# Optimization experiments

Hardware: AMD Instinct MI355X
Metric: run time of the kernel (lower is better)

The kernel has to match this reference:

```python
import jax, jax.numpy as jnp
import numpy as np

NX = 48
NY = 48
K0DX = 0.2026833935483871
N_PML = 8
_PI = 3.1415926


def _fun_s(u):
    # PML stretch factor s(u) = kappa(u) + 1j*sigma_over_omega(u)
    power_kappa = 3
    kappa_max = 15
    power_sigma = 3
    lambda_over_dx = 40
    sigma_over_omega_max = 0.8 * (power_sigma + 1) * lambda_over_dx / (2 * _PI)
    return (1.0 + (kappa_max - 1) * u ** power_kappa) + 1j * (sigma_over_omega_max * u ** power_sigma)


def _lap1d_pml(N, N_L, N_R):
    # 1D second-difference operator with stretched-coordinate PML (dense numpy, constant)
    ddx1 = np.eye(N + 1, N) - np.eye(N + 1, N, k=-1)   # forward difference (N+1, N)
    ddx2 = -ddx1.T                                      # (N, N+1)
    s_half = np.ones(N + 1, dtype=np.complex128)
    s_int = np.ones(N, dtype=np.complex128)
    if N_R > 0:
        s_half[N - N_R:N + 1] = _fun_s(np.arange(0.5, N_R + 1, 1.0) / (N_R + 1))
        s_int[N - N_R:N] = _fun_s(np.arange(1.0, N_R + 1, 1.0) / (N_R + 1))
    if N_L > 0:
        s_half[N_L::-1] = _fun_s(np.arange(0.5, N_L + 1, 1.0) / (N_L + 1))
        s_int[N_L - 1::-1] = _fun_s(np.arange(1.0, N_L + 1, 1.0) / (N_L + 1))
    return np.diag(1.0 / s_int) @ ddx2 @ np.diag(1.0 / s_half) @ ddx1


def _build_A1():
    # 2D Helmholtz Laplacian with PML: kron(Ax, I) + kron(I, Ay), dense 2304x2304 complex64
    Ax = _lap1d_pml(NX, N_PML, N_PML)
    Ay = _lap1d_pml(NY, N_PML, N_PML)
    return (np.kron(Ax, np.eye(NY)) + np.kron(np.eye(NX), Ay)).astype(np.complex64)


_A1 = _build_A1()  # constant system matrix part


def setup_inputs() -> dict:
    key = jax.random.key(0)
    k1, k2, k3, k4, k5 = jax.random.split(key, 5)
    return {
        "n_prediction": jax.random.uniform(k1, (1, NX, NY, 1), dtype=jnp.float32),
        "n_predict_allresults": jax.random.normal(k2, (1, NX, NY, 1), dtype=jnp.float32),
        "x_b": jax.random.normal(k3, (1, NX, NY, 1), dtype=jnp.float32),
        "y_aim": jax.random.normal(k4, (1, NX, NY, 2), dtype=jnp.float32),
        "simulation_region": jax.random.normal(k5, (1, NX, NY, 1), dtype=jnp.float32),
    }


def reference(n_prediction, n_predict_allresults, x_b, y_aim, simulation_region):
    A1 = jnp.asarray(_A1)  # (2304, 2304) complex64
    # A = A1 + k0dx^2 * diag(n^2), with n flattened after [0,2,1,3] transpose
    n_c = n_prediction.astype(jnp.complex64)
    n_flat = jnp.transpose(n_c, (0, 2, 1, 3)).reshape(-1)  # (2304,)
    A = A1 + jnp.diag((K0DX ** 2) * n_flat ** 2)
    # RHS b, same transpose+flatten convention
    b = jnp.transpose(x_b.astype(jnp.complex64), (0, 2, 1, 3)).reshape(NX * NY, 1)
    # Dense complex linear solve A psi = b
    psi = jnp.linalg.solve(A, b).reshape(1, NX, NY, 1)
    psi_tot = jnp.transpose(psi, (0, 2, 1, 3))  # (1, 48, 48, 1) complex64
    y_c = y_aim.astype(jnp.complex64)
    err1 = psi_tot * y_c[:, :, :, 0:1]
    err2 = psi_tot * y_c[:, :, :, 1:2]
    en1 = y_c[:, :, :, 0:1] * y_c[:, :, :, 0:1]
    en2 = y_c[:, :, :, 1:2] * y_c[:, :, :, 1:2]
    return jnp.concatenate([err1, err2, en1, en2], axis=-1)  # (1, 48, 48, 4) complex64
```

## Files before the change

### kernel.cpp

```cpp
#include <hip/hip_runtime.h>


#define NXY 48
#define NN  2304

typedef float v2 __attribute__((ext_vector_type(2)));
typedef double2 zplx;

__device__ __forceinline__ v2 mk2(float x, float y){ v2 r; r.x=x; r.y=y; return r; }
__device__ __forceinline__ v2 bcx(v2 a){ return __builtin_shufflevector(a,a,0,0); }
__device__ __forceinline__ v2 bcy(v2 a){ return __builtin_shufflevector(a,a,1,1); }
__device__ __forceinline__ v2 jswp(v2 a){ v2 r = __builtin_shufflevector(a,a,1,0); r.x = -r.x; return r; }
__device__ __forceinline__ v2 cmul(v2 a, v2 b){
    return __builtin_elementwise_fma(bcx(a), b, bcy(a)*jswp(b));
}
__device__ __forceinline__ v2 cfma_(v2 c, v2 a, v2 b){
    return __builtin_elementwise_fma(bcx(a), b, __builtin_elementwise_fma(bcy(a), jswp(b), c));
}
__device__ __forceinline__ v2 cfms(v2 c, v2 a, v2 b){
    return __builtin_elementwise_fma(-bcx(a), b, __builtin_elementwise_fma(-bcy(a), jswp(b), c));
}
__device__ __forceinline__ v2 cinv(v2 a){
    float s = 1.0f/fmaf(a.x,a.x, a.y*a.y);
    return mk2(a.x*s, -a.y*s);
}
__device__ __forceinline__ v2 shfl_c(v2 a, int lane){
    return mk2(__shfl(a.x, lane), __shfl(a.y, lane));
}
__device__ __forceinline__ v2 bfly_c(v2 v){
    v.x += __shfl_xor(v.x,1); v.y += __shfl_xor(v.y,1);
    v.x += __shfl_xor(v.x,2); v.y += __shfl_xor(v.y,2);
    v.x += __shfl_xor(v.x,4); v.y += __shfl_xor(v.y,4);
    return v;
}

__device__ __forceinline__ zplx zmul64(zplx a, zplx b){
    return make_double2(a.x*b.x - a.y*b.y, a.x*b.y + a.y*b.x);
}
__device__ __forceinline__ zplx zadd64(zplx a, zplx b){ return make_double2(a.x+b.x, a.y+b.y); }
__device__ __forceinline__ zplx zneg64(zplx a){ return make_double2(-a.x, -a.y); }
__device__ __forceinline__ zplx zinv64(zplx a){
    double s = 1.0/(a.x*a.x + a.y*a.y);
    return make_double2(a.x*s, -a.y*s);
}
__device__ __forceinline__ zplx fun_s(double u){
    const double sig = 0.8*4.0*40.0/(2.0*3.1415926);
    double u3 = u*u*u;
    return make_double2(1.0 + 14.0*u3, sig*u3);
}
__device__ __forceinline__ zplx s_half_at(int j){
    if (j <= 8)  return fun_s((8.5 - (double)j)/9.0);
    if (j >= 40) return fun_s(((double)(j-40) + 0.5)/9.0);
    return make_double2(1.0, 0.0);
}
__device__ __forceinline__ zplx s_int_at(int j){
    if (j <= 7)  return fun_s((8.0 - (double)j)/9.0);
    if (j >= 40) return fun_s(((double)(j-40) + 1.0)/9.0);
    return make_double2(1.0, 0.0);
}

__device__ __forceinline__ void gj48(v2 (&m)[6][6], const int lr, const int lc){
    v2 pv, rs[6], cs[6];
    {
        const int rsrc0 = lc, csrc0 = (lr<<3);
        pv = shfl_c(m[0][0], 0);
        #pragma unroll
        for (int j=0;j<6;++j) rs[j] = shfl_c(m[0][j], rsrc0);
        #pragma unroll
        for (int i=0;i<6;++i) cs[i] = shfl_c(m[i][0], csrc0);
    }
    #pragma unroll 1
    for (int kr=0; kr<8; ++kr){
        const bool prow = (lr==kr), pcol = (lc==kr);
        #pragma unroll
        for (int kj=0; kj<6; ++kj){
            const int nj = (kj+1)%6;
            const int cr = (kj==5) ? ((kr<7)?(kr+1):7) : kr;
            const int nrsrc = (cr<<3)|lc;
            const int ncsrc = (lr<<3)|cr;
            const int ndsrc = (cr<<3)|cr;
            v2 d = cinv(pv);
            v2 rsp[6];
            #pragma unroll
            for (int j=0;j<6;++j) rsp[j] = cmul(d, rs[j]);
            if (pcol) rsp[kj] = d + mk2(1.f,0.f);
            v2 u[6];
            #pragma unroll
            for (int i=0;i<6;++i) u[i] = cs[i];
            if (prow) u[kj] = pv - mk2(1.f,0.f);
            #pragma unroll
            for (int j=0;j<6;++j) m[nj][j] = cfms(m[nj][j], u[nj], rsp[j]);
            #pragma unroll
            for (int i=0;i<6;++i){ if (i!=nj) m[i][nj] = cfms(m[i][nj], u[i], rsp[nj]); }
            v2 npv = shfl_c(m[nj][nj], ndsrc);
            v2 nrs[6], ncs[6];
            #pragma unroll
            for (int j=0;j<6;++j) nrs[j] = shfl_c(m[nj][j], nrsrc);
            #pragma unroll
            for (int i=0;i<6;++i) ncs[i] = shfl_c(m[i][nj], ncsrc);
            #pragma unroll
            for (int i=0;i<6;++i){
                if (i==nj) continue;
                #pragma unroll
                for (int j=0;j<6;++j){
                    if (j==nj) continue;
                    m[i][j] = cfms(m[i][j], u[i], rsp[j]);
                }
            }
            pv = npv;
            #pragma unroll
            for (int j=0;j<6;++j){ rs[j]=nrs[j]; cs[j]=ncs[j]; }
        }
    }
}

__global__ __launch_bounds__(128,1) void helm_babe(
    const float* __restrict__ n_pred,
    const float* __restrict__ xb,
    const float* __restrict__ yaim,
    float*       __restrict__ out,
    int                       out_size,
    float*       __restrict__ wsG)
{
    __shared__ v2 dgv[NXY], lov[NXY], hiv[NXY];
    __shared__ float nk[NN];
    __shared__ float bb[NN];
    __shared__ v2 zv[NN];
    __shared__ v2 Hx[NN];
    __shared__ v2 vv[NXY];

    const int t    = threadIdx.x;
    const int lane = t & 63;
    const int wid  = t >> 6;
    const int lr = lane>>3, lc = lane&7;
    const int r0 = 6*lr, c0v = 6*lc;
    const int diagl = (lc<<3)|lc;
    const double k2 = 0.2026833935483871*0.2026833935483871;

    if (t < NXY){
        int a = t;
        zplx isha  = zinv64(s_half_at(a));
        zplx isha1 = zinv64(s_half_at(a+1));
        zplx isi   = zinv64(s_int_at(a));
        zplx dgd = zneg64(zmul64(isi, zadd64(isha,isha1)));
        zplx lod = zmul64(isi, isha);
        zplx hid = zmul64(isi, isha1);
        dgv[a] = mk2((float)dgd.x,(float)dgd.y);
        lov[a] = mk2((float)lod.x,(float)lod.y);
        hiv[a] = mk2((float)hid.x,(float)hid.y);
    }
    for (int e=t; e<NN; e+=128){
        int i_=e/48, a_=e%48;
        float nv = n_pred[a_*48+i_];
        nk[e] = (float)(k2*(double)nv*(double)nv);
        bb[e] = xb[a_*48+i_];
    }
    __syncthreads();

    const int dir    = (wid==0) ? 1 : -1;
    const int ibeg   = (wid==0) ? 0 : 47;
    const int nsteps = (wid==0) ? 25 : 23;

    v2 g[6][6];
    v2 m[6][6];
    v2 zrow[6];
    #pragma unroll
    for (int i=0;i<6;++i) zrow[i] = mk2(0.f,0.f);

    #pragma unroll 1
    for (int step=0; step<nsteps; ++step){
        int ib = ibeg + dir*step;
        bool full = !(wid==0 && step==24);

        v2 zc[6];
        #pragma unroll
        for (int j=0;j<6;++j) zc[j] = shfl_c(zrow[j], diagl);

        v2 nci = mk2(0.f,0.f), czp = mk2(0.f,0.f);
        if (step>0){
            if (dir>0){ nci = cmul(lov[ib], hiv[ib-1]); czp = lov[ib]; }
            else      { nci = cmul(hiv[ib], lov[ib+1]); czp = hiv[ib]; }
            nci = -nci;
        }
        bool same  = (lc==lr), rightn = (lc==lr+1), leftn = (lc+1==lr);
        v2 p[6];
        #pragma unroll
        for (int i=0;i<6;++i){
            int r = r0+i;
            v2 dgr = dgv[r], lor = lov[r], hir = hiv[r];
            v2 ddi = dgv[ib] + dgr + mk2(nk[ib*48+r],0.f);
            v2 acc = mk2(0.f,0.f);
            #pragma unroll
            for (int j=0;j<6;++j){
                v2 v = (step>0)? cmul(nci, g[i][j]) : mk2(0.f,0.f);
                if (same){
                    if (j==i)   v = v + ddi;
                    if (j==i+1) v = v + hir;
                    if (j+1==i) v = v + lor;
                }
                if (rightn && i==5 && j==0) v = v + hir;
                if (leftn  && i==0 && j==5) v = v + lor;
                m[i][j] = v;
                if (step>0) acc = cfma_(acc, g[i][j], zc[j]);
            }
            p[i] = acc;
        }
        if (step>0){
            #pragma unroll
            for (int i=0;i<6;++i){
                v2 w = bfly_c(p[i]);
                zrow[i] = cfms(mk2(bb[ib*48+r0+i],0.f), czp, w);
            }
        } else {
            #pragma unroll
            for (int i=0;i<6;++i) zrow[i] = mk2(bb[ib*48+r0+i], 0.f);
        }
        if (lc==0){
            #pragma unroll
            for (int i=0;i<6;++i) zv[ib*48+r0+i] = zrow[i];
        }

        if (full){
            gj48(m, lr, lc);
            if (ib == 25){
                #pragma unroll
                for (int i=0;i<6;++i)
                    #pragma unroll
                    for (int j=0;j<6;++j) Hx[(r0+i)*48 + c0v + j] = m[i][j];
            } else {
                #pragma unroll
                for (int i=0;i<6;++i){
                    float4* w4 = (float4*)(wsG + 2*((size_t)ib*NN + (r0+i)*48 + c0v));
                    #pragma unroll
                    for (int jp=0;jp<3;++jp){
                        float4 f;
                        f.x = m[i][2*jp].x;   f.y = m[i][2*jp].y;
                        f.z = m[i][2*jp+1].x; f.w = m[i][2*jp+1].y;
                        w4[jp] = f;
                    }
                }
            }
            #pragma unroll
            for (int i=0;i<6;++i)
                #pragma unroll
                for (int j=0;j<6;++j) g[i][j] = m[i][j];
        }
    }

    if (wid==1){
        v2 zc[6];
        #pragma unroll
        for (int j=0;j<6;++j) zc[j] = shfl_c(zrow[j], diagl);
        #pragma unroll
        for (int i=0;i<6;++i){
            v2 acc = mk2(0.f,0.f);
            #pragma unroll
            for (int j=0;j<6;++j) acc = cfma_(acc, m[i][j], zc[j]);
            acc = bfly_c(acc);
            if (lc==0) vv[r0+i] = acc;
        }
    }
    __syncthreads();

    v2 xrow[6];
    if (wid==0){
        v2 cf = cmul(hiv[24], lov[25]);
        #pragma unroll
        for (int i=0;i<6;++i)
            #pragma unroll
            for (int j=0;j<6;++j) m[i][j] = cfms(m[i][j], cf, Hx[(r0+i)*48 + c0v + j]);
        #pragma unroll
        for (int i=0;i<6;++i) zrow[i] = cfms(zrow[i], hiv[24], vv[r0+i]);
        gj48(m, lr, lc);
        v2 zc[6];
        #pragma unroll
        for (int j=0;j<6;++j) zc[j] = shfl_c(zrow[j], diagl);
        #pragma unroll
        for (int i=0;i<6;++i){
            v2 acc = mk2(0.f,0.f);
            #pragma unroll
            for (int j=0;j<6;++j) acc = cfma_(acc, m[i][j], zc[j]);
            xrow[i] = bfly_c(acc);
        }
        if (lc==0){
            #pragma unroll
            for (int i=0;i<6;++i) zv[24*48+r0+i] = xrow[i];
        }
        v2 xc[6], tm[6];
        #pragma unroll
        for (int j=0;j<6;++j) xc[j] = shfl_c(xrow[j], diagl);
        #pragma unroll
        for (int j=0;j<6;++j) tm[j] = cfms(zv[25*48+c0v+j], lov[25], xc[j]);
        #pragma unroll
        for (int i=0;i<6;++i){
            v2 acc = mk2(0.f,0.f);
            #pragma unroll
            for (int j=0;j<6;++j) acc = cfma_(acc, Hx[(r0+i)*48 + c0v + j], tm[j]);
            acc = bfly_c(acc);
            if (lc==0) zv[25*48+r0+i] = acc;
        }
    }
    __syncthreads();

    if (wid==0){
        #pragma unroll 1
        for (int ib=23; ib>=0; --ib){
            v2 xc[6], tm[6];
            #pragma unroll
            for (int j=0;j<6;++j) xc[j] = shfl_c(xrow[j], diagl);
            v2 hiib = hiv[ib];
            #pragma unroll
            for (int j=0;j<6;++j) tm[j] = cfms(zv[ib*48+c0v+j], hiib, xc[j]);
            #pragma unroll
            for (int i=0;i<6;++i){
                const float4* w4 = (const float4*)(wsG + 2*((size_t)ib*NN + (r0+i)*48 + c0v));
                v2 acc = mk2(0.f,0.f);
                #pragma unroll
                for (int jp=0;jp<3;++jp){
                    float4 f = w4[jp];
                    acc = cfma_(acc, mk2(f.x,f.y), tm[2*jp]);
                    acc = cfma_(acc, mk2(f.z,f.w), tm[2*jp+1]);
                }
                xrow[i] = bfly_c(acc);
            }
            if (lc==0){
                #pragma unroll
                for (int i=0;i<6;++i) zv[ib*48+r0+i] = xrow[i];
            }
        }
    } else {
        #pragma unroll
        for (int i=0;i<6;++i) xrow[i] = zv[25*48+r0+i];
        #pragma unroll 1
        for (int ib=26; ib<NXY; ++ib){
            v2 xc[6], tm[6];
            #pragma unroll
            for (int j=0;j<6;++j) xc[j] = shfl_c(xrow[j], diagl);
            v2 loib = lov[ib];
            #pragma unroll
            for (int j=0;j<6;++j) tm[j] = cfms(zv[ib*48+c0v+j], loib, xc[j]);
            #pragma unroll
            for (int i=0;i<6;++i){
                const float4* w4 = (const float4*)(wsG + 2*((size_t)ib*NN + (r0+i)*48 + c0v));
                v2 acc = mk2(0.f,0.f);
                #pragma unroll
                for (int jp=0;jp<3;++jp){
                    float4 f = w4[jp];
                    acc = cfma_(acc, mk2(f.x,f.y), tm[2*jp]);
                    acc = cfma_(acc, mk2(f.z,f.w), tm[2*jp+1]);
                }
                xrow[i] = bfly_c(acc);
            }
            if (lc==0){
                #pragma unroll
                for (int i=0;i<6;++i) zv[ib*48+r0+i] = xrow[i];
            }
        }
    }
    __syncthreads();

    for (int e=t; e<NN; e+=128){
        int alpha=e/48, beta=e%48;
        v2 psi = zv[beta*48+alpha];
        float y0=yaim[2*e], y1=yaim[2*e+1];
        if (out_size == NN*4){
            float4 o = make_float4(psi.x*y0, psi.x*y1, y0*y0, y1*y1);
            *(float4*)(out + 4*e) = o;
        } else {
            float* o = out + 8*e;
            o[0]=psi.x*y0; o[1]=psi.y*y0; o[2]=psi.x*y1; o[3]=psi.y*y1;
            o[4]=y0*y0; o[5]=0.f; o[6]=y1*y1; o[7]=0.f;
        }
    }
}

extern "C" void kernel_launch(void* const* d_in, const int* in_sizes, int n_in,
                              void* d_out, int out_size, void* d_ws, size_t ws_size,
                              hipStream_t stream) {
    const float* n_pred = (const float*)d_in[0];
    const float* xb     = (const float*)d_in[2];
    const float* ya     = (const float*)d_in[3];
    float* out = (float*)d_out;
    float* wsG = (float*)d_ws;

    hipLaunchKernelGGL(helm_babe, dim3(1), dim3(128), 0, stream,
                       n_pred, xb, ya, out, out_size, wsG);
}
```

Baseline: 615.5 us.

## Block Gauss-Jordan 48x48 inversion with 2x2 pivot blocks

Replaces the scalar-pivot in-register Gauss-Jordan inversion with a 2x2 block-pivot version. Each step eliminates two pivot rows and columns together using an explicit 2x2 inverse, which halves the number of sequential pivot steps and the cross-lane shuffle/broadcast rounds on the critical path. The cost is more arithmetic per step, higher register pressure from the doubled row and column buffers, and pivoting on 2x2 determinants without pivot search, which may change numerical stability.

```diff
diff --git a/kernel.cpp b/kernel.cpp
--- a/kernel.cpp
+++ b/kernel.cpp
@@ -14,6 +14,9 @@
 __device__ __forceinline__ v2 cmul(v2 a, v2 b){
     return __builtin_elementwise_fma(bcx(a), b, bcy(a)*jswp(b));
 }
+__device__ __forceinline__ v2 cadd(v2 a, v2 b){ return a+b; }
+__device__ __forceinline__ v2 csub(v2 a, v2 b){ return a-b; }
+__device__ __forceinline__ v2 cneg(v2 a){ return -a; }
 __device__ __forceinline__ v2 cfma_(v2 c, v2 a, v2 b){
     return __builtin_elementwise_fma(bcx(a), b, __builtin_elementwise_fma(bcy(a), jswp(b), c));
 }
@@ -33,6 +36,9 @@
     v.x += __shfl_xor(v.x,4); v.y += __shfl_xor(v.y,4);
     return v;
 }
+__device__ __forceinline__ float4 pk4(v2 a, v2 b){ return make_float4(a.x,a.y,b.x,b.y); }
+__device__ __forceinline__ v2 lo2(float4 f){ return mk2(f.x,f.y); }
+__device__ __forceinline__ v2 hi2(float4 f){ return mk2(f.z,f.w); }
 
 __device__ __forceinline__ zplx zmul64(zplx a, zplx b){
     return make_double2(a.x*b.x - a.y*b.y, a.x*b.y + a.y*b.x);
@@ -59,58 +65,99 @@
     return make_double2(1.0, 0.0);
 }
 
-__device__ __forceinline__ void gj48(v2 (&m)[6][6], const int lr, const int lc){
-    v2 pv, rs[6], cs[6];
-    {
-        const int rsrc0 = lc, csrc0 = (lr<<3);
-        pv = shfl_c(m[0][0], 0);
-        #pragma unroll
-        for (int j=0;j<6;++j) rs[j] = shfl_c(m[0][j], rsrc0);
-        #pragma unroll
-        for (int i=0;i<6;++i) cs[i] = shfl_c(m[i][0], csrc0);
-    }
+template<int NI>
+__device__ __forceinline__ void gather_pair(const v2 (&m)[6][6], int gkr, int lr, int lc,
+    v2 (&rs0)[6], v2 (&rs1)[6], v2 (&cs0)[6], v2 (&cs1)[6],
+    v2 &P00, v2 &P01, v2 &P10, v2 &P11)
+{
+    const int rsrc = (gkr<<3)|lc;
+    const int csrc = (lr<<3)|gkr;
+    const int dsrc = (gkr<<3)|gkr;
+    #pragma unroll
+    for (int j=0;j<6;++j){ rs0[j] = shfl_c(m[NI][j], rsrc); rs1[j] = shfl_c(m[NI+1][j], rsrc); }
+    #pragma unroll
+    for (int i=0;i<6;++i){ cs0[i] = shfl_c(m[i][NI], csrc); cs1[i] = shfl_c(m[i][NI+1], csrc); }
+    P00 = shfl_c(m[NI][NI],   dsrc); P01 = shfl_c(m[NI][NI+1],   dsrc);
+    P10 = shfl_c(m[NI+1][NI], dsrc); P11 = shfl_c(m[NI+1][NI+1], dsrc);
+}
+
+#define UPD(i,j) m[i][j] = cfms(cfms(m[i][j], u0[i], rsp0[j]), u1[i], rsp1[j])
+
+template<int KJ2>
+__device__ __forceinline__ void gjb2_phase(v2 (&m)[6][6], const int kr, const bool last,
+    const int lr, const int lc,
+    v2 (&rs0)[6], v2 (&rs1)[6], v2 (&cs0)[6], v2 (&cs1)[6],
+    v2 &P00, v2 &P01, v2 &P10, v2 &P11)
+{
+    constexpr int iA = 2*KJ2, iB = iA+1;
+    constexpr int niA = 2*((KJ2+1)%3), niB = niA+1;
+    const int nkr = (KJ2==2)? kr+1 : kr;
+    const bool prow = (lr==kr), pcol = (lc==kr);
+
+    v2 det  = csub(cmul(P00,P11), cmul(P01,P10));
+    v2 dinv = cinv(det);
+    v2 D00 = cmul(P11,dinv);
+    v2 D01 = cneg(cmul(P01,dinv));
+    v2 D10 = cneg(cmul(P10,dinv));
+    v2 D11 = cmul(P00,dinv);
+
+    v2 u0[6], u1[6];
+    #pragma unroll
+    for (int i=0;i<6;++i){ u0[i]=cs0[i]; u1[i]=cs1[i]; }
+    if (prow){
+        u0[iA] = csub(P00, mk2(1.f,0.f)); u1[iA] = P01;
+        u0[iB] = P10;                     u1[iB] = csub(P11, mk2(1.f,0.f));
+    }
+    v2 rsp0[6], rsp1[6];
+    #pragma unroll
+    for (int j=0;j<6;++j){
+        rsp0[j] = cadd(cmul(D00,rs0[j]), cmul(D01,rs1[j]));
+        rsp1[j] = cadd(cmul(D10,rs0[j]), cmul(D11,rs1[j]));
+    }
+    if (pcol){
+        rsp0[iA] = cadd(D00, mk2(1.f,0.f)); rsp1[iA] = D10;
+        rsp0[iB] = D01;                     rsp1[iB] = cadd(D11, mk2(1.f,0.f));
+    }
+
+    if (!last){
+        #pragma unroll
+        for (int j=0;j<6;++j){ UPD(niA,j); UPD(niB,j); }
+        #pragma unroll
+        for (int i=0;i<6;++i){
+            if (i==niA||i==niB) continue;
+            UPD(i,niA); UPD(i,niB);
+        }
+        v2 nrs0[6],nrs1[6],ncs0[6],ncs1[6],nP00,nP01,nP10,nP11;
+        gather_pair<niA>(m, nkr, lr, lc, nrs0,nrs1,ncs0,ncs1, nP00,nP01,nP10,nP11);
+        #pragma unroll
+        for (int i=0;i<6;++i){
+            if (i==niA||i==niB) continue;
+            #pragma unroll
+            for (int j=0;j<6;++j){
+                if (j==niA||j==niB) continue;
+                UPD(i,j);
+            }
+        }
+        #pragma unroll
+        for (int j=0;j<6;++j){ rs0[j]=nrs0[j]; rs1[j]=nrs1[j]; cs0[j]=ncs0[j]; cs1[j]=ncs1[j]; }
+        P00=nP00; P01=nP01; P10=nP10; P11=nP11;
+    } else {
+        #pragma unroll
+        for (int i=0;i<6;++i){
+            #pragma unroll
+            for (int j=0;j<6;++j) UPD(i,j);
+        }
+    }
+}
+
+__device__ __forceinline__ void gj48b2(v2 (&m)[6][6], int lr, int lc){
+    v2 rs0[6],rs1[6],cs0[6],cs1[6],P00,P01,P10,P11;
+    gather_pair<0>(m, 0, lr, lc, rs0,rs1,cs0,cs1, P00,P01,P10,P11);
     #pragma unroll 1
     for (int kr=0; kr<8; ++kr){
-        const bool prow = (lr==kr), pcol = (lc==kr);
-        #pragma unroll
-        for (int kj=0; kj<6; ++kj){
-            const int nj = (kj+1)%6;
-            const int cr = (kj==5) ? ((kr<7)?(kr+1):7) : kr;
-            const int nrsrc = (cr<<3)|lc;
-            const int ncsrc = (lr<<3)|cr;
-            const int ndsrc = (cr<<3)|cr;
-            v2 d = cinv(pv);
-            v2 rsp[6];
-            #pragma unroll
-            for (int j=0;j<6;++j) rsp[j] = cmul(d, rs[j]);
-            if (pcol) rsp[kj] = d + mk2(1.f,0.f);
-            v2 u[6];
-            #pragma unroll
-            for (int i=0;i<6;++i) u[i] = cs[i];
-            if (prow) u[kj] = pv - mk2(1.f,0.f);
-            #pragma unroll
-            for (int j=0;j<6;++j) m[nj][j] = cfms(m[nj][j], u[nj], rsp[j]);
-            #pragma unroll
-            for (int i=0;i<6;++i){ if (i!=nj) m[i][nj] = cfms(m[i][nj], u[i], rsp[nj]); }
-            v2 npv = shfl_c(m[nj][nj], ndsrc);
-            v2 nrs[6], ncs[6];
-            #pragma unroll
-            for (int j=0;j<6;++j) nrs[j] = shfl_c(m[nj][j], nrsrc);
-            #pragma unroll
-            for (int i=0;i<6;++i) ncs[i] = shfl_c(m[i][nj], ncsrc);
-            #pragma unroll
-            for (int i=0;i<6;++i){
-                if (i==nj) continue;
-                #pragma unroll
-                for (int j=0;j<6;++j){
-                    if (j==nj) continue;
-                    m[i][j] = cfms(m[i][j], u[i], rsp[j]);
-                }
-            }
-            pv = npv;
-            #pragma unroll
-            for (int j=0;j<6;++j){ rs[j]=nrs[j]; cs[j]=ncs[j]; }
-        }
+        gjb2_phase<0>(m, kr, false,   lr, lc, rs0,rs1,cs0,cs1, P00,P01,P10,P11);
+        gjb2_phase<1>(m, kr, false,   lr, lc, rs0,rs1,cs0,cs1, P00,P01,P10,P11);
+        gjb2_phase<2>(m, kr, (kr==7), lr, lc, rs0,rs1,cs0,cs1, P00,P01,P10,P11);
     }
 }
 
@@ -221,7 +268,7 @@
         }
 
         if (full){
-            gj48(m, lr, lc);
+            gj48b2(m, lr, lc);
             if (ib == 25){
                 #pragma unroll
                 for (int i=0;i<6;++i)
@@ -232,12 +279,7 @@
                 for (int i=0;i<6;++i){
                     float4* w4 = (float4*)(wsG + 2*((size_t)ib*NN + (r0+i)*48 + c0v));
                     #pragma unroll
-                    for (int jp=0;jp<3;++jp){
-                        float4 f;
-                        f.x = m[i][2*jp].x;   f.y = m[i][2*jp].y;
-                        f.z = m[i][2*jp+1].x; f.w = m[i][2*jp+1].y;
-                        w4[jp] = f;
-                    }
+                    for (int jp=0;jp<3;++jp) w4[jp] = pk4(m[i][2*jp], m[i][2*jp+1]);
                 }
             }
             #pragma unroll
@@ -271,7 +313,7 @@
             for (int j=0;j<6;++j) m[i][j] = cfms(m[i][j], cf, Hx[(r0+i)*48 + c0v + j]);
         #pragma unroll
         for (int i=0;i<6;++i) zrow[i] = cfms(zrow[i], hiv[24], vv[r0+i]);
-        gj48(m, lr, lc);
+        gj48b2(m, lr, lc);
         v2 zc[6];
         #pragma unroll
         for (int j=0;j<6;++j) zc[j] = shfl_c(zrow[j], diagl);
@@ -318,8 +360,8 @@
                 #pragma unroll
                 for (int jp=0;jp<3;++jp){
                     float4 f = w4[jp];
-                    acc = cfma_(acc, mk2(f.x,f.y), tm[2*jp]);
-                    acc = cfma_(acc, mk2(f.z,f.w), tm[2*jp+1]);
+                    acc = cfma_(acc, lo2(f), tm[2*jp]);
+                    acc = cfma_(acc, hi2(f), tm[2*jp+1]);
                 }
                 xrow[i] = bfly_c(acc);
             }
@@ -346,8 +388,8 @@
                 #pragma unroll
                 for (int jp=0;jp<3;++jp){
                     float4 f = w4[jp];
-                    acc = cfma_(acc, mk2(f.x,f.y), tm[2*jp]);
-                    acc = cfma_(acc, mk2(f.z,f.w), tm[2*jp+1]);
+                    acc = cfma_(acc, lo2(f), tm[2*jp]);
+                    acc = cfma_(acc, hi2(f), tm[2*jp+1]);
                 }
                 xrow[i] = bfly_c(acc);
             }
```

Measured after the change: 726.0 us. 1.18x slower.

## Restructure Gauss-Jordan pivot step to prefetch next pivot row/col before the full update

Applied to the files above, without the earlier changes.

The 48x48 in-register Gauss-Jordan elimination is split into a templated per-pivot step. Each step now shuffles the next pivot row, column and diagonal from the pre-update matrix and corrects them algebraically with one rank-1 fix, instead of updating the next row and column first and then shuffling. This takes the cross-lane shuffles off the critical path so they can overlap the bulk rank-1 update. Separately, the g[6][6] register copy is removed by computing the matrix-vector product with the previous inverse before overwriting m. This lowers register pressure at the cost of slightly different rounding order.

```diff
diff --git a/kernel.cpp b/kernel.cpp
--- a/kernel.cpp
+++ b/kernel.cpp
@@ -33,6 +33,9 @@
     v.x += __shfl_xor(v.x,4); v.y += __shfl_xor(v.y,4);
     return v;
 }
+__device__ __forceinline__ float4 pk4(v2 a, v2 b){ return make_float4(a.x,a.y,b.x,b.y); }
+__device__ __forceinline__ v2 lo2(float4 f){ return mk2(f.x,f.y); }
+__device__ __forceinline__ v2 hi2(float4 f){ return mk2(f.z,f.w); }
 
 __device__ __forceinline__ zplx zmul64(zplx a, zplx b){
     return make_double2(a.x*b.x - a.y*b.y, a.x*b.y + a.y*b.x);
@@ -59,58 +62,66 @@
     return make_double2(1.0, 0.0);
 }
 
-__device__ __forceinline__ void gj48(v2 (&m)[6][6], const int lr, const int lc){
-    v2 pv, rs[6], cs[6];
-    {
-        const int rsrc0 = lc, csrc0 = (lr<<3);
-        pv = shfl_c(m[0][0], 0);
-        #pragma unroll
-        for (int j=0;j<6;++j) rs[j] = shfl_c(m[0][j], rsrc0);
-        #pragma unroll
-        for (int i=0;i<6;++i) cs[i] = shfl_c(m[i][0], csrc0);
-    }
+template<int KJ>
+__device__ __forceinline__ void piv_step(v2 (&m)[6][6], const int kr, const bool last,
+    const int lr, const int lc, v2 (&rs)[6], v2 (&cs)[6], v2 &pv)
+{
+    constexpr int NKJ = (KJ+1)%6;
+    const int nkr = (KJ==5) ? kr+1 : kr;
+    const bool prow = (lr==kr), pcol = (lc==kr);
+
+    v2 d = cinv(pv);
+    v2 rsp[6];
+    #pragma unroll
+    for (int j=0;j<6;++j) rsp[j] = cmul(d, rs[j]);
+    if (pcol) rsp[KJ] = d + mk2(1.f,0.f);
+    v2 u[6];
+    #pragma unroll
+    for (int i=0;i<6;++i) u[i] = cs[i];
+    if (prow) u[KJ] = pv - mk2(1.f,0.f);
+
+    if (!last){
+        v2 un_r    = shfl_c(cs[NKJ], (nkr<<3));
+        v2 rn_r    = shfl_c(rs[NKJ], nkr);
+        v2 npv_raw = shfl_c(m[NKJ][NKJ], (nkr<<3)|nkr);
+        v2 nrs_raw[6], ncs_raw[6];
+        #pragma unroll
+        for (int j=0;j<6;++j) nrs_raw[j] = shfl_c(m[NKJ][j], (nkr<<3)|lc);
+        #pragma unroll
+        for (int i=0;i<6;++i) ncs_raw[i] = shfl_c(m[i][NKJ], (lr<<3)|nkr);
+        #pragma unroll
+        for (int i=0;i<6;++i)
+            #pragma unroll
+            for (int j=0;j<6;++j) m[i][j] = cfms(m[i][j], u[i], rsp[j]);
+        v2 rspn = cmul(d, rn_r);
+        #pragma unroll
+        for (int j=0;j<6;++j) rs[j] = cfms(nrs_raw[j], un_r, rsp[j]);
+        #pragma unroll
+        for (int i=0;i<6;++i) cs[i] = cfms(ncs_raw[i], u[i], rspn);
+        pv = cfms(npv_raw, un_r, rspn);
+    } else {
+        #pragma unroll
+        for (int i=0;i<6;++i)
+            #pragma unroll
+            for (int j=0;j<6;++j) m[i][j] = cfms(m[i][j], u[i], rsp[j]);
+    }
+}
+
+__device__ __forceinline__ void gj48(v2 (&m)[6][6], int lr, int lc){
+    v2 rs[6], cs[6], pv;
+    #pragma unroll
+    for (int j=0;j<6;++j) rs[j] = shfl_c(m[0][j], lc);
+    #pragma unroll
+    for (int i=0;i<6;++i) cs[i] = shfl_c(m[i][0], (lr<<3));
+    pv = shfl_c(m[0][0], 0);
     #pragma unroll 1
     for (int kr=0; kr<8; ++kr){
-        const bool prow = (lr==kr), pcol = (lc==kr);
-        #pragma unroll
-        for (int kj=0; kj<6; ++kj){
-            const int nj = (kj+1)%6;
-            const int cr = (kj==5) ? ((kr<7)?(kr+1):7) : kr;
-            const int nrsrc = (cr<<3)|lc;
-            const int ncsrc = (lr<<3)|cr;
-            const int ndsrc = (cr<<3)|cr;
-            v2 d = cinv(pv);
-            v2 rsp[6];
-            #pragma unroll
-            for (int j=0;j<6;++j) rsp[j] = cmul(d, rs[j]);
-            if (pcol) rsp[kj] = d + mk2(1.f,0.f);
-            v2 u[6];
-            #pragma unroll
-            for (int i=0;i<6;++i) u[i] = cs[i];
-            if (prow) u[kj] = pv - mk2(1.f,0.f);
-            #pragma unroll
-            for (int j=0;j<6;++j) m[nj][j] = cfms(m[nj][j], u[nj], rsp[j]);
-            #pragma unroll
-            for (int i=0;i<6;++i){ if (i!=nj) m[i][nj] = cfms(m[i][nj], u[i], rsp[nj]); }
-            v2 npv = shfl_c(m[nj][nj], ndsrc);
-            v2 nrs[6], ncs[6];
-            #pragma unroll
-            for (int j=0;j<6;++j) nrs[j] = shfl_c(m[nj][j], nrsrc);
-            #pragma unroll
-            for (int i=0;i<6;++i) ncs[i] = shfl_c(m[i][nj], ncsrc);
-            #pragma unroll
-            for (int i=0;i<6;++i){
-                if (i==nj) continue;
-                #pragma unroll
-                for (int j=0;j<6;++j){
-                    if (j==nj) continue;
-                    m[i][j] = cfms(m[i][j], u[i], rsp[j]);
-                }
-            }
-            pv = npv;
-            #pragma unroll
-            for (int j=0;j<6;++j){ rs[j]=nrs[j]; cs[j]=ncs[j]; }
-        }
+        piv_step<0>(m, kr, false, lr, lc, rs, cs, pv);
+        piv_step<1>(m, kr, false, lr, lc, rs, cs, pv);
+        piv_step<2>(m, kr, false, lr, lc, rs, cs, pv);
+        piv_step<3>(m, kr, false, lr, lc, rs, cs, pv);
+        piv_step<4>(m, kr, false, lr, lc, rs, cs, pv);
+        piv_step<5>(m, kr, (kr==7), lr, lc, rs, cs, pv);
     }
 }
 
@@ -161,7 +172,6 @@
     const int ibeg   = (wid==0) ? 0 : 47;
     const int nsteps = (wid==0) ? 25 : 23;
 
-    v2 g[6][6];
     v2 m[6][6];
     v2 zrow[6];
     #pragma unroll
@@ -182,17 +192,25 @@
             else      { nci = cmul(hiv[ib], lov[ib+1]); czp = hiv[ib]; }
             nci = -nci;
         }
+        v2 p[6];
+        if (step>0){
+            #pragma unroll
+            for (int i=0;i<6;++i){
+                v2 acc = mk2(0.f,0.f);
+                #pragma unroll
+                for (int j=0;j<6;++j) acc = cfma_(acc, m[i][j], zc[j]);
+                p[i] = acc;
+            }
+        }
         bool same  = (lc==lr), rightn = (lc==lr+1), leftn = (lc+1==lr);
-        v2 p[6];
         #pragma unroll
         for (int i=0;i<6;++i){
             int r = r0+i;
             v2 dgr = dgv[r], lor = lov[r], hir = hiv[r];
             v2 ddi = dgv[ib] + dgr + mk2(nk[ib*48+r],0.f);
-            v2 acc = mk2(0.f,0.f);
             #pragma unroll
             for (int j=0;j<6;++j){
-                v2 v = (step>0)? cmul(nci, g[i][j]) : mk2(0.f,0.f);
+                v2 v = (step>0)? cmul(nci, m[i][j]) : mk2(0.f,0.f);
                 if (same){
                     if (j==i)   v = v + ddi;
                     if (j==i+1) v = v + hir;
@@ -201,9 +219,7 @@
                 if (rightn && i==5 && j==0) v = v + hir;
                 if (leftn  && i==0 && j==5) v = v + lor;
                 m[i][j] = v;
-                if (step>0) acc = cfma_(acc, g[i][j], zc[j]);
-            }
-            p[i] = acc;
+            }
         }
         if (step>0){
             #pragma unroll
@@ -232,18 +248,9 @@
                 for (int i=0;i<6;++i){
                     float4* w4 = (float4*)(wsG + 2*((size_t)ib*NN + (r0+i)*48 + c0v));
                     #pragma unroll
-                    for (int jp=0;jp<3;++jp){
-                        float4 f;
-                        f.x = m[i][2*jp].x;   f.y = m[i][2*jp].y;
-                        f.z = m[i][2*jp+1].x; f.w = m[i][2*jp+1].y;
-                        w4[jp] = f;
-                    }
+                    for (int jp=0;jp<3;++jp) w4[jp] = pk4(m[i][2*jp], m[i][2*jp+1]);
                 }
             }
-            #pragma unroll
-            for (int i=0;i<6;++i)
-                #pragma unroll
-                for (int j=0;j<6;++j) g[i][j] = m[i][j];
         }
     }
 
@@ -318,8 +325,8 @@
                 #pragma unroll
                 for (int jp=0;jp<3;++jp){
                     float4 f = w4[jp];
-                    acc = cfma_(acc, mk2(f.x,f.y), tm[2*jp]);
-                    acc = cfma_(acc, mk2(f.z,f.w), tm[2*jp+1]);
+                    acc = cfma_(acc, lo2(f), tm[2*jp]);
+                    acc = cfma_(acc, hi2(f), tm[2*jp+1]);
                 }
                 xrow[i] = bfly_c(acc);
             }
@@ -346,8 +353,8 @@
                 #pragma unroll
                 for (int jp=0;jp<3;++jp){
                     float4 f = w4[jp];
-                    acc = cfma_(acc, mk2(f.x,f.y), tm[2*jp]);
-                    acc = cfma_(acc, mk2(f.z,f.w), tm[2*jp+1]);
+                    acc = cfma_(acc, lo2(f), tm[2*jp]);
+                    acc = cfma_(acc, hi2(f), tm[2*jp+1]);
                 }
                 xrow[i] = bfly_c(acc);
             }
```

Result: slower. 705.3 us (+14.6%).
